# Performance work log

Hardware: AMD Instinct MI355X
Metric: run time of the kernel (lower is better)

## Reference

```python
import jax, jax.numpy as jnp
import numpy as np

V, E, H, S, B = 50000, 128, 256, 400, 128
MAX_OOV = 50

def _lin(x, W, b=None):
    y = x @ W.T
    return y if b is None else y + b

def setup_inputs() -> dict:
    key = jax.random.key(0)
    ks = iter(jax.random.split(key, 32))
    def rn(shape, scale=0.05):
        return (jax.random.normal(next(ks), shape, dtype=jnp.float32) * scale)
    inp = {
        'decoder_input_one_step': jax.random.randint(next(ks), (B,), 0, V),
        'h0': rn((B, H), 1.0), 'c0': rn((B, H), 1.0),
        'encoder_output': rn((B, S, 2 * H), 1.0),
        'encoder_mask': jnp.ones((B, S), dtype=jnp.int32),
        'context_vec': rn((B, 2 * H), 1.0),
        'oovs_zero': jnp.zeros((B, MAX_OOV), dtype=jnp.float32),
        'encoder_with_oov': jax.random.randint(next(ks), (B, S), 0, V + MAX_OOV),
        'coverage': jnp.zeros((B, S), dtype=jnp.float32),
    }
    # parameters (torch layout: Linear weight [out, in])
    emb = rn((V, E)).at[0].set(0.0)  # padding_idx=0
    params = {
        'emb': emb,
        'Wi': rn((E, 2 * H + E)), 'bi': rn((E,)),
        'W_ih': rn((4 * H, E)), 'W_hh': rn((4 * H, H)), 'b_ih': rn((4 * H,)), 'b_hh': rn((4 * H,)),
        'att_wh': rn((2 * H, 2 * H)), 'att_ws': rn((2 * H, 2 * H)),
        'att_wc': rn((2 * H, 1)), 'att_bc': rn((2 * H,)), 'att_v': rn((1, 2 * H)),
        'gp_wh': rn((1, 2 * H)), 'gp_bh': rn((1,)),
        'gp_ws': rn((1, 2 * H)), 'gp_bs': rn((1,)),
        'gp_wx': rn((1, E)), 'gp_bx': rn((1,)),
        'out_w1': rn((H, 3 * H)), 'out_b1': rn((H,)),
        'out_w2': rn((V, H)), 'out_b2': rn((V,)),
    }
    inp.update(params)
    return inp

def reference(decoder_input_one_step, h0, c0, encoder_output, encoder_mask,
              context_vec, oovs_zero, encoder_with_oov, coverage,
              emb, Wi, bi, W_ih, W_hh, b_ih, b_hh,
              att_wh, att_ws, att_wc, att_bc, att_v,
              gp_wh, gp_bh, gp_ws, gp_bs, gp_wx, gp_bx,
              out_w1, out_b1, out_w2, out_b2):
    # embedding + lstm input projection
    embed = emb[decoder_input_one_step]                      # [B,E]
    x = _lin(jnp.concatenate([context_vec, embed], -1), Wi, bi)  # [B,E]
    # single-step LSTM cell (torch gate order i,f,g,o)
    gates = x @ W_ih.T + b_ih + h0 @ W_hh.T + b_hh           # [B,4H]
    i, f, g, o = jnp.split(gates, 4, axis=-1)
    c_t = jax.nn.sigmoid(f) * c0 + jax.nn.sigmoid(i) * jnp.tanh(g)
    h_t = jax.nn.sigmoid(o) * jnp.tanh(c_t)                  # [B,H]
    status = jnp.concatenate([h_t, c_t], -1)                 # [B,2H]
    # additive attention with coverage
    enc_feat = encoder_output @ att_wh.T                     # [B,S,2H]
    dec_feat = (status @ att_ws.T)[:, None, :]               # [B,1,2H]
    cov_feat = coverage[:, :, None] * att_wc[:, 0] + att_bc  # [B,S,2H]
    e_t = jnp.tanh(enc_feat + dec_feat + cov_feat) @ att_v[0]  # [B,S]
    e_t = jnp.where(encoder_mask == 0, -jnp.inf, e_t)
    a_t = jax.nn.softmax(e_t, axis=-1)                       # [B,S]
    next_coverage = coverage + a_t
    ctx = jnp.einsum('bs,bsd->bd', a_t, encoder_output)      # [B,2H]
    # generation probability
    gen_p = jax.nn.sigmoid(_lin(ctx, gp_wh, gp_bh) + _lin(status, gp_ws, gp_bs)
                           + _lin(x, gp_wx, gp_bx))          # [B,1]
    # output MLP + vocab softmax
    out_feat = jnp.concatenate([h_t, ctx], -1)               # [B,3H]
    logits = _lin(jax.nn.relu(_lin(out_feat, out_w1, out_b1)), out_w2, out_b2)
    vocab_dist = jax.nn.softmax(logits, axis=-1)             # [B,V]
    # pointer-generator scatter-add combine
    vocab_dist_p = jnp.concatenate([vocab_dist * gen_p, oovs_zero], -1)  # [B,V+OOV]
    context_dist_p = a_t * (1.0 - gen_p)                     # [B,S]
    rows = jnp.arange(vocab_dist_p.shape[0])[:, None]
    final_dist = vocab_dist_p.at[rows, encoder_with_oov].add(context_dist_p)
    return final_dist, h_t, c_t, ctx, a_t, gen_p, next_coverage
```

## Files before the change

kernel.cpp:

```cpp
#include <hip/hip_runtime.h>
#include <hip/hip_bf16.h>
#include <string.h>

#define V_    50000
#define VO_   50050
#define E_    128
#define H_    256
#define S_    400
#define B_    128
#define OOV_  50

typedef __bf16  bf16x8 __attribute__((ext_vector_type(8)));
typedef float   f32x4  __attribute__((ext_vector_type(4)));
typedef unsigned short u16;
typedef unsigned int   u32;

__device__ __forceinline__ float sigm(float x){ return 1.f/(1.f+__expf(-x)); }
__device__ __forceinline__ float tanh_fast(float x){ float e = __expf(2.f*x); return 1.f - 2.f/(e+1.f); }
__device__ __forceinline__ u16 f2bits(float f){ __hip_bfloat16 h = __float2bfloat16(f); u16 b; memcpy(&b, &h, 2); return b; }

#define ASYNC_COPY16(g, l) \
    __builtin_amdgcn_global_load_lds((const __attribute__((address_space(1))) u32*)(g), \
                                     (__attribute__((address_space(3))) u32*)(l), 16, 0, 0)

__global__ void k_init(float* p, int n){
    int i = blockIdx.x*256 + threadIdx.x;
    if (i < n) p[i] = 0.f;
}

__global__ void k_cvt(const float* src, u16* dst){
    int i = (blockIdx.x*256 + threadIdx.x) * 4;
    float4 v = *(const float4*)&src[i];
    ushort4 pk = { f2bits(v.x), f2bits(v.y), f2bits(v.z), f2bits(v.w) };
    *(ushort4*)&dst[i] = pk;
}

__global__ void k_small1(const int* tok, const float* emb, const float* ctxv,
                         const float* h0, const float* c0,
                         const float* Wi, const float* bi,
                         const float* W_ih, const float* W_hh,
                         const float* b_ih, const float* b_hh,
                         const float* aws,
                         float* o_ht, float* o_ct,
                         float* ws_status, float* ws_x, float* ws_dec)
{
    int b = blockIdx.x, t = threadIdx.x;
    __shared__ float in_vec[640];
    __shared__ float h0s[256];
    __shared__ float xs[128];
    __shared__ float xred[256];
    __shared__ float gates[1024];
    __shared__ float st[512];
    for (int i = t; i < 512; i += 256) in_vec[i] = ctxv[b*512+i];
    int tk = tok[b];
    if (t < 128) in_vec[512+t] = emb[tk*128+t];
    h0s[t] = h0[b*256+t];
    __syncthreads();
    {
        int row = t >> 1, half = t & 1;
        float s = 0.f;
        const float* wr = Wi + row*640 + half*320;
        const float* iv = in_vec + half*320;
        for (int k = 0; k < 320; k++) s += wr[k] * iv[k];
        xred[t] = s;
    }
    __syncthreads();
    if (t < 128) {
        float s = xred[2*t] + xred[2*t+1] + bi[t];
        xs[t] = s; ws_x[b*128+t] = s;
    }
    __syncthreads();
    for (int g = t; g < 1024; g += 256) {
        float s = b_ih[g] + b_hh[g];
        const float* wr = W_ih + g*128;
        for (int k = 0; k < 128; k++) s += wr[k] * xs[k];
        const float* hr = W_hh + g*256;
        for (int k = 0; k < 256; k++) s += hr[k] * h0s[k];
        gates[g] = s;
    }
    __syncthreads();
    {
        float ig = sigm(gates[t]);
        float fg = sigm(gates[256+t]);
        float gg = tanhf(gates[512+t]);
        float og = sigm(gates[768+t]);
        float c  = fg * c0[b*256+t] + ig * gg;
        float h  = og * tanhf(c);
        st[t] = h; st[256+t] = c;
        o_ht[b*256+t] = h; o_ct[b*256+t] = c;
        ws_status[b*512+t] = h; ws_status[b*512+256+t] = c;
    }
    __syncthreads();
    for (int d = t; d < 512; d += 256) {
        float s = 0.f;
        const float* wr = aws + d*512;
        for (int k = 0; k < 512; k++) s += wr[k] * st[k];
        ws_dec[b*512+d] = s;
    }
}

__global__ __launch_bounds__(256, 2) void k_attn(
    const float* enc, const u16* whb, const float* dec, const float* cov,
    const float* wc, const float* bc, const float* vv, float* e_t)
{
    const int M0 = blockIdx.x * 64;
    const int N0 = blockIdx.y * 256;
    int t = threadIdx.x;
    int wave = t >> 6, lane = t & 63, quad = lane >> 4, l16 = lane & 15;
    __shared__ __align__(16) u16 As[64*40];
    __shared__ __align__(16) u16 Bs[256*32];
    f32x4 acc[4][4] = {};
    const int arow = t >> 2, ac8 = (t & 3) * 8;
    const int brow_l = (lane >> 2);
    const int bkk  = (lane & 3) * 8;
    for (int kt = 0; kt < 512; kt += 32) {
        #pragma unroll
        for (int j = 0; j < 4; j++) {
            int rbase = wave*64 + j*16;
            const u16* src = whb + (size_t)(N0 + rbase + brow_l)*512 + kt + bkk;
            ASYNC_COPY16(src, &Bs[rbase*32]);
        }
        {
            const float* ap = &enc[(size_t)(M0 + arow)*512 + kt + ac8];
            float4 v0 = *(const float4*)ap;
            float4 v1 = *(const float4*)(ap + 4);
            ushort4 p0 = { f2bits(v0.x), f2bits(v0.y), f2bits(v0.z), f2bits(v0.w) };
            ushort4 p1 = { f2bits(v1.x), f2bits(v1.y), f2bits(v1.z), f2bits(v1.w) };
            *(ushort4*)&As[arow*40 + ac8]     = p0;
            *(ushort4*)&As[arow*40 + ac8 + 4] = p1;
        }
        __syncthreads();
        bf16x8 af[4], bfr[4];
        #pragma unroll
        for (int mi = 0; mi < 4; mi++)
            af[mi] = *(const bf16x8*)&As[(mi*16 + l16)*40 + quad*8];
        #pragma unroll
        for (int ni = 0; ni < 4; ni++)
            bfr[ni] = *(const bf16x8*)&Bs[(wave*64 + ni*16 + l16)*32 + quad*8];
        #pragma unroll
        for (int mi = 0; mi < 4; mi++)
            #pragma unroll
            for (int ni = 0; ni < 4; ni++)
                acc[mi][ni] = __builtin_amdgcn_mfma_f32_16x16x32_bf16(af[mi], bfr[ni], acc[mi][ni], 0, 0, 0);
        __syncthreads();
    }
    #pragma unroll
    for (int mi = 0; mi < 4; mi++) {
        #pragma unroll
        for (int rr = 0; rr < 4; rr++) {
            int rl = mi*16 + quad*4 + rr;
            int row = M0 + rl;
            int bb = row / 400;
            float covv = cov[row];
            float psum = 0.f;
            #pragma unroll
            for (int ni = 0; ni < 4; ni++) {
                int d = N0 + wave*64 + ni*16 + l16;
                float arg = acc[mi][ni][rr] + dec[bb*512 + d] + covv * wc[d] + bc[d];
                psum += vv[d] * tanh_fast(arg);
            }
            psum += __shfl_xor(psum, 1);
            psum += __shfl_xor(psum, 2);
            psum += __shfl_xor(psum, 4);
            psum += __shfl_xor(psum, 8);
            if (l16 == 0) atomicAdd(&e_t[row], psum);
        }
    }
}

__global__ void k_softmax_s(const float* e_t, const int* mask, const float* cov,
                            float* a_ws, float* o_at, float* o_cov)
{
    int b = blockIdx.x, t = threadIdx.x;
    __shared__ float red[256];
    __shared__ float vals[400];
    float m = -1e30f;
    for (int s = t; s < 400; s += 256) {
        float v = (mask[b*400+s] == 0) ? -1e30f : e_t[b*400+s];
        vals[s] = v;
        m = fmaxf(m, v);
    }
    red[t] = m; __syncthreads();
    for (int o = 128; o > 0; o >>= 1) { if (t < o) red[t] = fmaxf(red[t], red[t+o]); __syncthreads(); }
    m = red[0]; __syncthreads();
    float sum = 0.f;
    for (int s = t; s < 400; s += 256) { float e = __expf(vals[s]-m); vals[s] = e; sum += e; }
    red[t] = sum; __syncthreads();
    for (int o = 128; o > 0; o >>= 1) { if (t < o) red[t] += red[t+o]; __syncthreads(); }
    float inv = 1.f / red[0];
    for (int s = t; s < 400; s += 256) {
        float a = vals[s] * inv;
        a_ws[b*400+s] = a;
        o_at[b*400+s] = a;
        o_cov[b*400+s] = cov[b*400+s] + a;
    }
}

__global__ void k_ctx(const float* a_ws, const float* enc, float* ctx_ws)
{
    int b = blockIdx.x, t = threadIdx.x;
    int s0 = blockIdx.y * 50;
    float acc0 = 0.f, acc1 = 0.f;
    for (int s = s0; s < s0+50; s++) {
        float a = a_ws[b*400+s];
        const float* er = enc + ((size_t)b*400 + s)*512;
        float2 v = *(const float2*)&er[2*t];
        acc0 += a * v.x;
        acc1 += a * v.y;
    }
    atomicAdd(&ctx_ws[b*512 + 2*t],     acc0);
    atomicAdd(&ctx_ws[b*512 + 2*t + 1], acc1);
}

__global__ void k_small2(const float* ctx_ws, const float* status, const float* x_ws,
                         const float* gp_wh, const float* gp_bh,
                         const float* gp_ws_, const float* gp_bs,
                         const float* gp_wx, const float* gp_bx,
                         const float* w1, const float* b1,
                         float* o_ctx, float* o_gp,
                         float* gp_v, u16* out1)
{
    int b = blockIdx.x, t = threadIdx.x;
    __shared__ float feat[768];
    __shared__ float red[256];
    feat[t] = status[b*512+t];
    for (int i = t; i < 512; i += 256) {
        float c = ctx_ws[b*512+i];
        feat[256+i] = c;
        o_ctx[b*512+i] = c;
    }
    __syncthreads();
    float p = 0.f;
    for (int k = t; k < 512; k += 256) {
        p += gp_wh[k]  * feat[256+k];
        p += gp_ws_[k] * status[b*512+k];
    }
    if (t < 128) p += gp_wx[t] * x_ws[b*128+t];
    red[t] = p; __syncthreads();
    for (int o = 128; o > 0; o >>= 1) { if (t < o) red[t] += red[t+o]; __syncthreads(); }
    if (t == 0) {
        float gp = sigm(red[0] + gp_bh[0] + gp_bs[0] + gp_bx[0]);
        gp_v[b] = gp; o_gp[b] = gp;
    }
    __syncthreads();
    {
        float s = b1[t];
        const float* wr = w1 + t*768;
        for (int k = 0; k < 768; k++) s += wr[k] * feat[k];
        out1[b*256+t] = f2bits(fmaxf(s, 0.f));
    }
}

__global__ __launch_bounds__(256) void k_logits(const u16* out1, const float* w2,
                                                const float* b2, float* o_fin)
{
    const int N0 = blockIdx.x * 64;
    int t = threadIdx.x, wave = t >> 6, lane = t & 63, quad = lane >> 4, l16 = lane & 15;
    __shared__ __align__(16) u16 As[128*40];
    __shared__ __align__(16) u16 Bs[64*40];
    f32x4 acc[2][4] = {};
    for (int kt = 0; kt < 256; kt += 32) {
        #pragma unroll
        for (int j = 0; j < 2; j++) {
            int gi = j*256 + t;
            int row = gi >> 2, c = gi & 3;
            *(uint4*)&As[row*40 + c*8] = *(const uint4*)&out1[row*256 + kt + c*8];
        }
        #pragma unroll
        for (int j = 0; j < 2; j++) {
            int gi = j*256 + t;
            int col = gi >> 3, c4 = gi & 7;
            int n = N0 + col;
            float4 v = (n < V_) ? *(const float4*)&w2[(size_t)n*256 + kt + c4*4]
                                : make_float4(0.f,0.f,0.f,0.f);
            ushort4 pk = { f2bits(v.x), f2bits(v.y), f2bits(v.z), f2bits(v.w) };
            *(ushort4*)&Bs[col*40 + c4*4] = pk;
        }
        __syncthreads();
        bf16x8 af[2], bfr[4];
        #pragma unroll
        for (int mi = 0; mi < 2; mi++)
            af[mi] = *(const bf16x8*)&As[(wave*32 + mi*16 + l16)*40 + quad*8];
        #pragma unroll
        for (int ni = 0; ni < 4; ni++)
            bfr[ni] = *(const bf16x8*)&Bs[(ni*16 + l16)*40 + quad*8];
        #pragma unroll
        for (int mi = 0; mi < 2; mi++)
            #pragma unroll
            for (int ni = 0; ni < 4; ni++)
                acc[mi][ni] = __builtin_amdgcn_mfma_f32_16x16x32_bf16(af[mi], bfr[ni], acc[mi][ni], 0, 0, 0);
        __syncthreads();
    }
    #pragma unroll
    for (int ni = 0; ni < 4; ni++) {
        int n = N0 + ni*16 + l16;
        if (n < V_) {
            float bias = b2[n];
            #pragma unroll
            for (int mi = 0; mi < 2; mi++) {
                #pragma unroll
                for (int rr = 0; rr < 4; rr++) {
                    int row = wave*32 + mi*16 + quad*4 + rr;
                    o_fin[(size_t)row*VO_ + n] = acc[mi][ni][rr] + bias;
                }
            }
        }
    }
}

__global__ void k_rowstats(const float* o_fin, float* pm, float* ps)
{
    int b = blockIdx.x, q = blockIdx.y, t = threadIdx.x;
    int i0 = q * 6250, i1 = i0 + 6250;
    float m = -1e30f, s = 0.f;
    const float* lr = o_fin + (size_t)b*VO_;
    for (int i = i0 + t; i < i1; i += 256) {
        float x = lr[i];
        if (x > m) { s = s * __expf(m - x) + 1.f; m = x; }
        else       { s += __expf(x - m); }
    }
    __shared__ float ms[256], ss[256];
    ms[t] = m; ss[t] = s; __syncthreads();
    for (int o = 128; o > 0; o >>= 1) {
        if (t < o) {
            float m2 = fmaxf(ms[t], ms[t+o]);
            ss[t] = ss[t]*__expf(ms[t]-m2) + ss[t+o]*__expf(ms[t+o]-m2);
            ms[t] = m2;
        }
        __syncthreads();
    }
    if (t == 0) { pm[b*8+q] = ms[0]; ps[b*8+q] = ss[0]; }
}

__global__ void k_norm(float* o_fin, const float* pm, const float* ps,
                       const float* gp, const float* oovz)
{
    int b = blockIdx.y;
    int i = blockIdx.x*256 + threadIdx.x;
    if (i >= VO_) return;
    float m = -1e30f;
    #pragma unroll
    for (int q = 0; q < 8; q++) m = fmaxf(m, pm[b*8+q]);
    float s = 0.f;
    #pragma unroll
    for (int q = 0; q < 8; q++) s += ps[b*8+q] * __expf(pm[b*8+q] - m);
    size_t idx = (size_t)b*VO_ + i;
    if (i < V_) {
        float l = o_fin[idx];
        o_fin[idx] = __expf(l - m) * (gp[b] / s);
    } else {
        o_fin[idx] = oovz[b*OOV_ + (i - V_)];
    }
}

__global__ void k_scatter(const int* eoov, const float* a_ws, const float* gp,
                          float* o_fin)
{
    int b = blockIdx.x, t = threadIdx.x;
    float w = 1.f - gp[b];
    for (int s = t; s < 400; s += 256) {
        int idx = eoov[b*400+s];
        float v = a_ws[b*400+s] * w;
        atomicAdd(&o_fin[(size_t)b*VO_ + idx], v);
    }
}

extern "C" void kernel_launch(void* const* d_in, const int* in_sizes, int n_in,
                              void* d_out, int out_size, void* d_ws, size_t ws_size,
                              hipStream_t stream)
{
    const int*   tok  = (const int*)d_in[0];
    const float* h0   = (const float*)d_in[1];
    const float* c0   = (const float*)d_in[2];
    const float* enc  = (const float*)d_in[3];
    const int*   mask = (const int*)d_in[4];
    const float* ctxv = (const float*)d_in[5];
    const float* oovz = (const float*)d_in[6];
    const int*   eoov = (const int*)d_in[7];
    const float* cov  = (const float*)d_in[8];
    const float* emb  = (const float*)d_in[9];
    const float* Wi   = (const float*)d_in[10];
    const float* bi   = (const float*)d_in[11];
    const float* W_ih = (const float*)d_in[12];
    const float* W_hh = (const float*)d_in[13];
    const float* b_ih = (const float*)d_in[14];
    const float* b_hh = (const float*)d_in[15];
    const float* awh  = (const float*)d_in[16];
    const float* aws  = (const float*)d_in[17];
    const float* awc  = (const float*)d_in[18];
    const float* abc  = (const float*)d_in[19];
    const float* av   = (const float*)d_in[20];
    const float* gp_wh= (const float*)d_in[21];
    const float* gp_bh= (const float*)d_in[22];
    const float* gp_ws= (const float*)d_in[23];
    const float* gp_bs= (const float*)d_in[24];
    const float* gp_wx= (const float*)d_in[25];
    const float* gp_bx= (const float*)d_in[26];
    const float* w1   = (const float*)d_in[27];
    const float* b1   = (const float*)d_in[28];
    const float* w2   = (const float*)d_in[29];
    const float* b2   = (const float*)d_in[30];

    char* ws = (char*)d_ws;
    float* ctx_ws = (float*)(ws + 0);
    float* e_t    = (float*)(ws + 262144);
    float* status = (float*)(ws + 466944);
    float* x_ws   = (float*)(ws + 729088);
    float* dec_ws = (float*)(ws + 794624);
    float* a_ws   = (float*)(ws + 1056768);
    float* gp_v   = (float*)(ws + 1261568);
    u16*   out1   = (u16*)  (ws + 1263104);
    u16*   wh_bf  = (u16*)  (ws + 1328640);
    float* pm     = (float*)(ws + 1852928);
    float* psum   = (float*)(ws + 1857024);

    float* out   = (float*)d_out;
    float* o_fin = out;
    float* o_ht  = out + 6406400;
    float* o_ct  = out + 6439168;
    float* o_ctx = out + 6471936;
    float* o_at  = out + 6537472;
    float* o_gp  = out + 6588672;
    float* o_cov = out + 6588800;

    k_init<<<dim3(457), 256, 0, stream>>>((float*)ws, 116736);
    k_cvt<<<dim3(256), 256, 0, stream>>>(awh, wh_bf);
    k_small1<<<dim3(128), 256, 0, stream>>>(tok, emb, ctxv, h0, c0, Wi, bi,
                                            W_ih, W_hh, b_ih, b_hh, aws,
                                            o_ht, o_ct, status, x_ws, dec_ws);
    k_attn<<<dim3(800, 2), 256, 0, stream>>>(enc, wh_bf, dec_ws, cov, awc, abc, av, e_t);
    k_softmax_s<<<dim3(128), 256, 0, stream>>>(e_t, mask, cov, a_ws, o_at, o_cov);
    k_ctx<<<dim3(128, 8), 256, 0, stream>>>(a_ws, enc, ctx_ws);
    k_small2<<<dim3(128), 256, 0, stream>>>(ctx_ws, status, x_ws,
                                            gp_wh, gp_bh, gp_ws, gp_bs, gp_wx, gp_bx,
                                            w1, b1, o_ctx, o_gp, gp_v, out1);
    k_logits<<<dim3(782), 256, 0, stream>>>(out1, w2, b2, o_fin);
    k_rowstats<<<dim3(128, 8), 256, 0, stream>>>(o_fin, pm, psum);
    k_norm<<<dim3(196, 128), 256, 0, stream>>>(o_fin, pm, psum, gp_v, oovz);
    k_scatter<<<dim3(128), 256, 0, stream>>>(eoov, a_ws, gp_v, o_fin);
}
```

Baseline: 542.3 us.

## Split serial per-batch small GEMVs into wave-per-output kernels with coalesced weight reads

The monolithic per-batch k_small1 kernel, in which each thread walked a whole weight row with strided uncoalesced reads across only 128 blocks, is split into four kernels: input projection, LSTM gates, cell update and decoder feature. Each GEMV kernel assigns one wavefront per output element, reads weights coalesced across lanes and finishes with a shuffle reduction. The same treatment moves the out_w1 projection out of k_small2 into a new k_out1 kernel. The aim is to remove the low-occupancy, latency-bound serial dot products, at the cost of more kernel launches, a gates workspace round trip, and weights re-read once per batch row.

```diff
diff --git a/kernel.cpp b/kernel.cpp
--- a/kernel.cpp
+++ b/kernel.cpp
@@ -19,6 +19,12 @@
 __device__ __forceinline__ float tanh_fast(float x){ float e = __expf(2.f*x); return 1.f - 2.f/(e+1.f); }
 __device__ __forceinline__ u16 f2bits(float f){ __hip_bfloat16 h = __float2bfloat16(f); u16 b; memcpy(&b, &h, 2); return b; }
 
+__device__ __forceinline__ float wave_reduce(float s){
+    s += __shfl_xor(s, 1);  s += __shfl_xor(s, 2);  s += __shfl_xor(s, 4);
+    s += __shfl_xor(s, 8);  s += __shfl_xor(s, 16); s += __shfl_xor(s, 32);
+    return s;
+}
+
 #define ASYNC_COPY16(g, l) \
     __builtin_amdgcn_global_load_lds((const __attribute__((address_space(1))) u32*)(g), \
                                      (__attribute__((address_space(3))) u32*)(l), 16, 0, 0)
@@ -35,68 +41,75 @@
     *(ushort4*)&dst[i] = pk;
 }
 
-__global__ void k_small1(const int* tok, const float* emb, const float* ctxv,
-                         const float* h0, const float* c0,
-                         const float* Wi, const float* bi,
-                         const float* W_ih, const float* W_hh,
-                         const float* b_ih, const float* b_hh,
-                         const float* aws,
-                         float* o_ht, float* o_ct,
-                         float* ws_status, float* ws_x, float* ws_dec)
+__global__ __launch_bounds__(1024) void k_x(const int* tok, const float* emb, const float* ctxv,
+                                            const float* Wi, const float* bi, float* x_ws)
+{
+    int t = threadIdx.x, lane = t & 63;
+    int gw = blockIdx.x*16 + (t >> 6);
+    int b = gw >> 7, n = gw & 127;
+    int tk = tok[b];
+    float s = 0.f;
+    #pragma unroll
+    for (int j = 0; j < 10; j++) {
+        int k = lane + j*64;
+        float a = (k < 512) ? ctxv[b*512 + k] : emb[tk*128 + (k - 512)];
+        s += a * Wi[n*640 + k];
+    }
+    s = wave_reduce(s);
+    if (lane == 0) x_ws[b*128 + n] = s + bi[n];
+}
+
+__global__ __launch_bounds__(1024) void k_gates(const float* x_ws, const float* h0,
+                                                const float* W_ih, const float* W_hh,
+                                                const float* b_ih, const float* b_hh,
+                                                float* gates_ws)
+{
+    int t = threadIdx.x, lane = t & 63;
+    int gw = blockIdx.x*16 + (t >> 6);
+    int b = gw >> 10, n = gw & 1023;
+    float s = 0.f;
+    #pragma unroll
+    for (int j = 0; j < 2; j++) {
+        int k = lane + j*64;
+        s += x_ws[b*128 + k] * W_ih[n*128 + k];
+    }
+    #pragma unroll
+    for (int j = 0; j < 4; j++) {
+        int k = lane + j*64;
+        s += h0[b*256 + k] * W_hh[n*256 + k];
+    }
+    s = wave_reduce(s);
+    if (lane == 0) gates_ws[b*1024 + n] = s + b_ih[n] + b_hh[n];
+}
+
+__global__ void k_lstm(const float* gates_ws, const float* c0,
+                       float* o_ht, float* o_ct, float* ws_status)
 {
     int b = blockIdx.x, t = threadIdx.x;
-    __shared__ float in_vec[640];
-    __shared__ float h0s[256];
-    __shared__ float xs[128];
-    __shared__ float xred[256];
-    __shared__ float gates[1024];
-    __shared__ float st[512];
-    for (int i = t; i < 512; i += 256) in_vec[i] = ctxv[b*512+i];
-    int tk = tok[b];
-    if (t < 128) in_vec[512+t] = emb[tk*128+t];
-    h0s[t] = h0[b*256+t];
-    __syncthreads();
-    {
-        int row = t >> 1, half = t & 1;
-        float s = 0.f;
-        const float* wr = Wi + row*640 + half*320;
-        const float* iv = in_vec + half*320;
-        for (int k = 0; k < 320; k++) s += wr[k] * iv[k];
-        xred[t] = s;
-    }
-    __syncthreads();
-    if (t < 128) {
-        float s = xred[2*t] + xred[2*t+1] + bi[t];
-        xs[t] = s; ws_x[b*128+t] = s;
-    }
-    __syncthreads();
-    for (int g = t; g < 1024; g += 256) {
-        float s = b_ih[g] + b_hh[g];
-        const float* wr = W_ih + g*128;
-        for (int k = 0; k < 128; k++) s += wr[k] * xs[k];
-        const float* hr = W_hh + g*256;
-        for (int k = 0; k < 256; k++) s += hr[k] * h0s[k];
-        gates[g] = s;
-    }
-    __syncthreads();
-    {
-        float ig = sigm(gates[t]);
-        float fg = sigm(gates[256+t]);
-        float gg = tanhf(gates[512+t]);
-        float og = sigm(gates[768+t]);
-        float c  = fg * c0[b*256+t] + ig * gg;
-        float h  = og * tanhf(c);
-        st[t] = h; st[256+t] = c;
-        o_ht[b*256+t] = h; o_ct[b*256+t] = c;
-        ws_status[b*512+t] = h; ws_status[b*512+256+t] = c;
-    }
-    __syncthreads();
-    for (int d = t; d < 512; d += 256) {
-        float s = 0.f;
-        const float* wr = aws + d*512;
-        for (int k = 0; k < 512; k++) s += wr[k] * st[k];
-        ws_dec[b*512+d] = s;
-    }
+    const float* g = gates_ws + b*1024;
+    float ig = sigm(g[t]);
+    float fg = sigm(g[256+t]);
+    float gg = tanhf(g[512+t]);
+    float og = sigm(g[768+t]);
+    float c  = fg * c0[b*256+t] + ig * gg;
+    float h  = og * tanhf(c);
+    o_ht[b*256+t] = h; o_ct[b*256+t] = c;
+    ws_status[b*512+t] = h; ws_status[b*512+256+t] = c;
+}
+
+__global__ __launch_bounds__(1024) void k_dec(const float* status, const float* aws, float* dec_ws)
+{
+    int t = threadIdx.x, lane = t & 63;
+    int gw = blockIdx.x*16 + (t >> 6);
+    int b = gw >> 9, n = gw & 511;
+    float s = 0.f;
+    #pragma unroll
+    for (int j = 0; j < 8; j++) {
+        int k = lane + j*64;
+        s += status[b*512 + k] * aws[n*512 + k];
+    }
+    s = wave_reduce(s);
+    if (lane == 0) dec_ws[b*512 + n] = s;
 }
 
 __global__ __launch_bounds__(256, 2) void k_attn(
@@ -216,23 +229,15 @@
                          const float* gp_wh, const float* gp_bh,
                          const float* gp_ws_, const float* gp_bs,
                          const float* gp_wx, const float* gp_bx,
-                         const float* w1, const float* b1,
-                         float* o_ctx, float* o_gp,
-                         float* gp_v, u16* out1)
+                         float* o_ctx, float* o_gp, float* gp_v)
 {
     int b = blockIdx.x, t = threadIdx.x;
-    __shared__ float feat[768];
     __shared__ float red[256];
-    feat[t] = status[b*512+t];
-    for (int i = t; i < 512; i += 256) {
-        float c = ctx_ws[b*512+i];
-        feat[256+i] = c;
-        o_ctx[b*512+i] = c;
-    }
-    __syncthreads();
     float p = 0.f;
     for (int k = t; k < 512; k += 256) {
-        p += gp_wh[k]  * feat[256+k];
+        float c = ctx_ws[b*512+k];
+        o_ctx[b*512+k] = c;
+        p += gp_wh[k]  * c;
         p += gp_ws_[k] * status[b*512+k];
     }
     if (t < 128) p += gp_wx[t] * x_ws[b*128+t];
@@ -242,13 +247,23 @@
         float gp = sigm(red[0] + gp_bh[0] + gp_bs[0] + gp_bx[0]);
         gp_v[b] = gp; o_gp[b] = gp;
     }
-    __syncthreads();
-    {
-        float s = b1[t];
-        const float* wr = w1 + t*768;
-        for (int k = 0; k < 768; k++) s += wr[k] * feat[k];
-        out1[b*256+t] = f2bits(fmaxf(s, 0.f));
-    }
+}
+
+__global__ __launch_bounds__(1024) void k_out1(const float* status, const float* ctx_ws,
+                                               const float* w1, const float* b1, u16* out1)
+{
+    int t = threadIdx.x, lane = t & 63;
+    int gw = blockIdx.x*16 + (t >> 6);
+    int b = gw >> 8, n = gw & 255;
+    float s = 0.f;
+    #pragma unroll
+    for (int j = 0; j < 12; j++) {
+        int k = lane + j*64;
+        float a = (k < 256) ? status[b*512 + k] : ctx_ws[b*512 + (k - 256)];
+        s += a * w1[n*768 + k];
+    }
+    s = wave_reduce(s);
+    if (lane == 0) out1[b*256 + n] = f2bits(fmaxf(s + b1[n], 0.f));
 }
 
 __global__ __launch_bounds__(256) void k_logits(const u16* out1, const float* w2,
@@ -402,17 +417,18 @@
     const float* b2   = (const float*)d_in[30];
 
     char* ws = (char*)d_ws;
-    float* ctx_ws = (float*)(ws + 0);
-    float* e_t    = (float*)(ws + 262144);
-    float* status = (float*)(ws + 466944);
-    float* x_ws   = (float*)(ws + 729088);
-    float* dec_ws = (float*)(ws + 794624);
-    float* a_ws   = (float*)(ws + 1056768);
-    float* gp_v   = (float*)(ws + 1261568);
-    u16*   out1   = (u16*)  (ws + 1263104);
-    u16*   wh_bf  = (u16*)  (ws + 1328640);
-    float* pm     = (float*)(ws + 1852928);
-    float* psum   = (float*)(ws + 1857024);
+    float* ctx_ws   = (float*)(ws + 0);
+    float* e_t      = (float*)(ws + 262144);
+    float* status   = (float*)(ws + 466944);
+    float* x_ws     = (float*)(ws + 729088);
+    float* dec_ws   = (float*)(ws + 794624);
+    float* a_ws     = (float*)(ws + 1056768);
+    float* gp_v     = (float*)(ws + 1261568);
+    u16*   out1     = (u16*)  (ws + 1263104);
+    u16*   wh_bf    = (u16*)  (ws + 1328640);
+    float* pm       = (float*)(ws + 1852928);
+    float* psum     = (float*)(ws + 1857024);
+    float* gates_ws = (float*)(ws + 1861120);
 
     float* out   = (float*)d_out;
     float* o_fin = out;
@@ -425,15 +441,17 @@
 
     k_init<<<dim3(457), 256, 0, stream>>>((float*)ws, 116736);
     k_cvt<<<dim3(256), 256, 0, stream>>>(awh, wh_bf);
-    k_small1<<<dim3(128), 256, 0, stream>>>(tok, emb, ctxv, h0, c0, Wi, bi,
-                                            W_ih, W_hh, b_ih, b_hh, aws,
-                                            o_ht, o_ct, status, x_ws, dec_ws);
+    k_x<<<dim3(1024), 1024, 0, stream>>>(tok, emb, ctxv, Wi, bi, x_ws);
+    k_gates<<<dim3(8192), 1024, 0, stream>>>(x_ws, h0, W_ih, W_hh, b_ih, b_hh, gates_ws);
+    k_lstm<<<dim3(128), 256, 0, stream>>>(gates_ws, c0, o_ht, o_ct, status);
+    k_dec<<<dim3(4096), 1024, 0, stream>>>(status, aws, dec_ws);
     k_attn<<<dim3(800, 2), 256, 0, stream>>>(enc, wh_bf, dec_ws, cov, awc, abc, av, e_t);
     k_softmax_s<<<dim3(128), 256, 0, stream>>>(e_t, mask, cov, a_ws, o_at, o_cov);
     k_ctx<<<dim3(128, 8), 256, 0, stream>>>(a_ws, enc, ctx_ws);
     k_small2<<<dim3(128), 256, 0, stream>>>(ctx_ws, status, x_ws,
                                             gp_wh, gp_bh, gp_ws, gp_bs, gp_wx, gp_bx,
-                                            w1, b1, o_ctx, o_gp, gp_v, out1);
+                                            o_ctx, o_gp, gp_v);
+    k_out1<<<dim3(2048), 1024, 0, stream>>>(status, ctx_ws, w1, b1, out1);
     k_logits<<<dim3(782), 256, 0, stream>>>(out1, w2, b2, o_fin);
     k_rowstats<<<dim3(128, 8), 256, 0, stream>>>(o_fin, pm, psum);
     k_norm<<<dim3(196, 128), 256, 0, stream>>>(o_fin, pm, psum, gp_v, oovz);
```

Measured after the change: 450.3 us. 1.2x faster.
